# Performance work log

Measured on AMD Instinct MI355X. Metric: run time of the kernel, lower is better.

## Reference

```python
import jax, jax.numpy as jnp
import numpy as np

B, S, D, H, FF = 16, 1024, 1024, 8, 4096
DH = D // H
EPS = 1e-5

def _ln(x, g, b):
    mu = jnp.mean(x, axis=-1, keepdims=True)
    var = jnp.mean((x - mu) ** 2, axis=-1, keepdims=True)
    return (x - mu) * jax.lax.rsqrt(var + EPS) * g + b

def setup_inputs() -> dict:
    key = jax.random.key(0)
    ks = jax.random.split(key, 12)
    sd = D ** -0.5
    return {
        "x": jax.random.normal(ks[0], (B, S, D), jnp.float32),
        "bias": jax.random.normal(ks[1], (S, S), jnp.float32),
        "Wq": jax.random.normal(ks[2], (D, D), jnp.float32) * sd,
        "bq": jnp.zeros((D,), jnp.float32),
        "Wk": jax.random.normal(ks[3], (D, D), jnp.float32) * sd,
        "bk": jnp.zeros((D,), jnp.float32),
        "Wv": jax.random.normal(ks[4], (D, D), jnp.float32) * sd,
        "bv": jnp.zeros((D,), jnp.float32),
        "Wo": jax.random.normal(ks[5], (D, D), jnp.float32) * sd,
        "bo": jnp.zeros((D,), jnp.float32),
        "ln1_g": jnp.ones((D,), jnp.float32),
        "ln1_b": jnp.zeros((D,), jnp.float32),
        "W1": jax.random.normal(ks[6], (FF, D), jnp.float32) * sd,
        "b1": jnp.zeros((FF,), jnp.float32),
        "W2": jax.random.normal(ks[7], (D, FF), jnp.float32) * (FF ** -0.5),
        "b2": jnp.zeros((D,), jnp.float32),
        "ln2_g": jnp.ones((D,), jnp.float32),
        "ln2_b": jnp.zeros((D,), jnp.float32),
    }

def reference(x, bias, Wq, bq, Wk, bk, Wv, bv, Wo, bo, ln1_g, ln1_b,
              W1, b1, W2, b2, ln2_g, ln2_b):
    # torch nn.Linear: y = x @ W.T + b
    Q = x @ Wq.T + bq  # [B,S,D]
    K = x @ Wk.T + bk
    V = x @ Wv.T + bv
    # Faithful to torch: plain row-major reshape [B,S,H*dh] -> [B*H,S,dh]
    Q = Q.reshape(B * H, S, DH)
    K = K.reshape(B * H, S, DH)
    V = V.reshape(B * H, S, DH)
    scale = DH ** -0.5
    scores = jnp.einsum('bqd,bkd->bqk', Q, K)  # [B*H,S,S]
    scores = (scores + bias[None]) * scale      # bias added BEFORE scaling, as in source
    attn = jax.nn.softmax(scores, axis=-1)
    selfattention = attn[0]
    ctx = jnp.einsum('bqk,bkd->bqd', attn, V).reshape(B, S, D)
    out = ctx @ Wo.T + bo
    out = _ln(out + x, ln1_g, ln1_b)
    # FFN
    h = jax.nn.relu(out @ W1.T + b1)
    ff = h @ W2.T + b2
    out2 = _ln(ff + out, ln2_g, ln2_b)
    return out2, selfattention
```

## Files before the change

kernel.cpp:

```cpp
#include <hip/hip_runtime.h>
#include <hip/hip_bf16.h>
#include <math.h>

typedef __attribute__((ext_vector_type(4))) float f32x4;
typedef __attribute__((ext_vector_type(8))) __bf16 bf16x8;
typedef __attribute__((ext_vector_type(4))) __bf16 bf16x4;

static constexpr float SCALE = 0.08838834764831845f;
static constexpr float SCALE_LOG2E = 0.1275174482f;

__device__ __forceinline__ void load_lds16(const void* g, void* l) {
  __builtin_amdgcn_global_load_lds(
      (const __attribute__((address_space(1))) void*)g,
      (__attribute__((address_space(3))) void*)l, 16, 0, 0);
}

__global__ __launch_bounds__(256) void cast_kernel(const float* __restrict__ s,
                                                   __bf16* __restrict__ d, int n4) {
  int i = blockIdx.x * blockDim.x + threadIdx.x;
  int stride = gridDim.x * blockDim.x;
  for (; i < n4; i += stride) {
    float4 v = reinterpret_cast<const float4*>(s)[i];
    bf16x4 o;
    o[0] = (__bf16)v.x; o[1] = (__bf16)v.y; o[2] = (__bf16)v.z; o[3] = (__bf16)v.w;
    reinterpret_cast<bf16x4*>(d)[i] = o;
  }
}

__global__ __launch_bounds__(256) void scale_cast_kernel(const float* __restrict__ s,
                                                         __bf16* __restrict__ d, int n4) {
  int i = blockIdx.x * blockDim.x + threadIdx.x;
  int stride = gridDim.x * blockDim.x;
  for (; i < n4; i += stride) {
    float4 v = reinterpret_cast<const float4*>(s)[i];
    bf16x4 o;
    o[0] = (__bf16)(v.x * SCALE_LOG2E); o[1] = (__bf16)(v.y * SCALE_LOG2E);
    o[2] = (__bf16)(v.z * SCALE_LOG2E); o[3] = (__bf16)(v.w * SCALE_LOG2E);
    reinterpret_cast<bf16x4*>(d)[i] = o;
  }
}

template <int EPI>
__global__ __launch_bounds__(512, 2) void gemm_bt(
    const __bf16* __restrict__ A, const __bf16* __restrict__ Bw,
    const float* __restrict__ bvec, __bf16* __restrict__ Cb,
    float* __restrict__ Cf, int M, int N, int K) {
  __shared__ __align__(16) char sm[131072];

  const int ntn = N >> 8;
  const int nwg = gridDim.x;
  const int bid = blockIdx.x;
  const int b = (bid & 7) * (nwg >> 3) + (bid >> 3);
  const int tm = b / ntn, tn = b % ntn;
  const int t = threadIdx.x, lane = t & 63;
  const int w = t >> 6;
  const int wm = w >> 2, wn = w & 3;
  const int l15 = lane & 15, lq = lane >> 4;

  f32x4 acc[8][4] = {};

  const int r0 = t >> 3;
  const int r1 = r0 + 64;
  const int kb0 = (((t & 7) << 4) ^ ((r0 & 7) << 4));
  const int wbase = w << 10;

  auto stage = [&](int kt, int p) {
    char* base = sm + (p << 16);
    const size_t kofs = (size_t)(kb0 >> 1) + ((size_t)kt << 6);
#pragma unroll
    for (int h = 0; h < 2; ++h) {
      const __bf16* gA = A + (size_t)((tm << 8) + (h << 7) + r0) * K + kofs;
      const __bf16* gA2 = A + (size_t)((tm << 8) + (h << 7) + r1) * K + kofs;
      char* lA = base + (h << 14) + wbase;
      load_lds16(gA, lA);
      load_lds16(gA2, lA + 8192);
      const __bf16* gB = Bw + (size_t)((tn << 8) + (h << 7) + r0) * K + kofs;
      const __bf16* gB2 = Bw + (size_t)((tn << 8) + (h << 7) + r1) * K + kofs;
      char* lB = base + 32768 + (h << 14) + wbase;
      load_lds16(gB, lB);
      load_lds16(gB2, lB + 8192);
    }
  };

  stage(0, 0);
  __syncthreads();

  const int NT = K >> 6;
  const int rbB = (wn & 1) << 6;
  for (int kt = 0; kt < NT; ++kt) {
    const int p = kt & 1;
    const char* Ab = sm + (p << 16) + (wm << 14);
    const char* Bb = sm + (p << 16) + 32768 + ((wn >> 1) << 14);
    if (kt + 1 < NT) stage(kt + 1, p ^ 1);

    bf16x8 bfv[4][2];
#pragma unroll
    for (int nf = 0; nf < 4; ++nf) {
      const int r = rbB + (nf << 4) + l15;
      const int sw = (r & 7) << 4;
#pragma unroll
      for (int ks = 0; ks < 2; ++ks) {
        const int lb = (ks << 6) + (lq << 4);
        bfv[nf][ks] = *(const bf16x8*)(Bb + r * 128 + (lb ^ sw));
      }
    }
#pragma unroll
    for (int q = 0; q < 4; ++q) {
      bf16x8 af[2][2];
#pragma unroll
      for (int dm = 0; dm < 2; ++dm) {
        const int r = (((q << 1) + dm) << 4) + l15;
        const int sw = (r & 7) << 4;
#pragma unroll
        for (int ks = 0; ks < 2; ++ks) {
          const int lb = (ks << 6) + (lq << 4);
          af[dm][ks] = *(const bf16x8*)(Ab + r * 128 + (lb ^ sw));
        }
      }
#pragma unroll
      for (int ks = 0; ks < 2; ++ks)
#pragma unroll
        for (int dm = 0; dm < 2; ++dm)
#pragma unroll
          for (int nf = 0; nf < 4; ++nf)
            acc[(q << 1) + dm][nf] = __builtin_amdgcn_mfma_f32_16x16x32_bf16(
                af[dm][ks], bfv[nf][ks], acc[(q << 1) + dm][nf], 0, 0, 0);
    }
    __syncthreads();
  }

  const int row0 = (tm << 8) + (wm << 7) + (lq << 2);
  const int col0 = (tn << 8) + (wn << 6) + l15;
#pragma unroll
  for (int nf = 0; nf < 4; ++nf) {
    const int col = col0 + (nf << 4);
    const float bv = bvec[col];
#pragma unroll
    for (int mf = 0; mf < 8; ++mf) {
#pragma unroll
      for (int r = 0; r < 4; ++r) {
        const int row = row0 + (mf << 4) + r;
        float v = acc[mf][nf][r] + bv;
        if (EPI == 1) v = fmaxf(v, 0.f);
        if (EPI == 2) {
          Cf[(size_t)row * N + col] = v;
        } else if (EPI == 3) {
          size_t vt = ((size_t)(row >> 7) << 17) + ((size_t)(col & 127) << 10) +
                      ((row & 127) << 3) + (col >> 7);
          Cb[vt] = (__bf16)v;
        } else {
          Cb[(size_t)row * N + col] = (__bf16)v;
        }
      }
    }
  }
}

__global__ __launch_bounds__(256) void attn_flash(
    const __bf16* __restrict__ Q, const __bf16* __restrict__ K,
    const __bf16* __restrict__ VT, const __bf16* __restrict__ biasS,
    __bf16* __restrict__ ctx) {
  __shared__ __bf16 Ks[64 * 128];
  __shared__ __bf16 VTs[128 * 64];
  __shared__ __bf16 Ps[4][16 * 64];

  const int bid = blockIdx.x;
  const int b = ((bid & 7) << 8) | (bid >> 3);
  const int g = b >> 4;
  const int q0 = (b & 15) << 6;
  const size_t goff = (size_t)g << 17;
  const __bf16* Qg = Q + goff;
  const __bf16* Kg = K + goff;
  const __bf16* VTg = VT + goff;

  const int t = threadIdx.x, w = t >> 6, lane = t & 63;
  const int l15 = lane & 15, lq = lane >> 4;
  const int qg = q0 + (w << 4) + l15;

  bf16x8 qf[4];
  {
    const __bf16* qrow = Qg + (size_t)qg * 128 + (lq << 3);
#pragma unroll
    for (int ec = 0; ec < 4; ++ec) qf[ec] = *(const bf16x8*)(qrow + (ec << 5));
  }
  const __bf16* bSr = biasS + ((size_t)qg << 10) + (lq << 2);

  float mrun = -INFINITY, lrun = 0.f;
  f32x4 cacc[8] = {};

  for (int kb = 0; kb < 1024; kb += 64) {
    {
      int srow = lane >> 4;
      int sbo = (lane & 15) << 4;
#pragma unroll
      for (int i = 0; i < 4; ++i) {
        int c = (w << 2) + i;
        int r = (c << 2) + srow;
        int ke = (sbo ^ ((r & 7) << 4)) >> 1;
        load_lds16(Kg + (size_t)(kb + r) * 128 + ke, (char*)Ks + (c << 10));
      }
    }
    {
      int srow = lane >> 3;
      int sbo = (lane & 7) << 4;
#pragma unroll
      for (int i = 0; i < 4; ++i) {
        int c = (w << 2) + i;
        int e = (c << 3) + srow;
        int ke = kb + ((sbo ^ ((e & 7) << 4)) >> 1);
        load_lds16(VTg + (size_t)e * 1024 + ke, (char*)VTs + (c << 10));
      }
    }
    __syncthreads();

    f32x4 sacc[4] = {};
    __builtin_amdgcn_s_setprio(1);
#pragma unroll
    for (int ec = 0; ec < 4; ++ec) {
      const int lb = (ec << 6) + (lq << 4);
#pragma unroll
      for (int kn = 0; kn < 4; ++kn) {
        int rb = (kn << 4) + l15;
        bf16x8 kf = *(const bf16x8*)((const char*)Ks + rb * 256 + (lb ^ ((rb & 7) << 4)));
        sacc[kn] = __builtin_amdgcn_mfma_f32_16x16x32_bf16(kf, qf[ec], sacc[kn], 0, 0, 0);
      }
    }
    __builtin_amdgcn_s_setprio(0);

    float sv[4][4];
    const __bf16* bt = bSr + kb;
#pragma unroll
    for (int kn = 0; kn < 4; ++kn) {
      bf16x4 bb = *(const bf16x4*)(bt + (kn << 4));
#pragma unroll
      for (int r = 0; r < 4; ++r)
        sv[kn][r] = fmaf(sacc[kn][r], SCALE_LOG2E, (float)bb[r]);
    }
    float mt = sv[0][0];
#pragma unroll
    for (int kn = 0; kn < 4; ++kn)
#pragma unroll
      for (int r = 0; r < 4; ++r) mt = fmaxf(mt, sv[kn][r]);
    mt = fmaxf(mt, __shfl_xor(mt, 16));
    mt = fmaxf(mt, __shfl_xor(mt, 32));

    float alpha = 1.f;
    if (__any(mt > mrun)) {
      float mnew = fmaxf(mrun, mt);
      alpha = exp2f(mrun - mnew);
      mrun = mnew;
      float alphaR[4];
#pragma unroll
      for (int r = 0; r < 4; ++r)
        alphaR[r] = __shfl(alpha, (lane & 48) + ((lane & 48) >> 2) + r);
#pragma unroll
      for (int et = 0; et < 8; ++et)
#pragma unroll
        for (int r = 0; r < 4; ++r) cacc[et][r] *= alphaR[r];
    }
    float psum = 0.f;
#pragma unroll
    for (int kn = 0; kn < 4; ++kn)
#pragma unroll
      for (int r = 0; r < 4; ++r) {
        float p = exp2f(sv[kn][r] - mrun);
        sv[kn][r] = p;
        psum += p;
      }
    psum += __shfl_xor(psum, 16);
    psum += __shfl_xor(psum, 32);
    lrun = lrun * alpha + psum;

#pragma unroll
    for (int kn = 0; kn < 4; ++kn) {
      bf16x4 pk;
      pk[0] = (__bf16)sv[kn][0]; pk[1] = (__bf16)sv[kn][1];
      pk[2] = (__bf16)sv[kn][2]; pk[3] = (__bf16)sv[kn][3];
      int bo = (kn << 5) + (lq << 3);
      *(bf16x4*)((char*)Ps[w] + l15 * 128 + (bo ^ ((l15 & 7) << 4))) = pk;
    }
    asm volatile("s_waitcnt lgkmcnt(0)" ::: "memory");
    __builtin_amdgcn_sched_barrier(0);

    __builtin_amdgcn_s_setprio(1);
#pragma unroll
    for (int ks = 0; ks < 2; ++ks) {
      const int lb = (ks << 6) + (lq << 4);
      bf16x8 paf = *(const bf16x8*)((const char*)Ps[w] + l15 * 128 + (lb ^ ((l15 & 7) << 4)));
#pragma unroll
      for (int et = 0; et < 8; ++et) {
        int e = (et << 4) + l15;
        bf16x8 vf = *(const bf16x8*)((const char*)VTs + e * 128 + (lb ^ ((e & 7) << 4)));
        cacc[et] = __builtin_amdgcn_mfma_f32_16x16x32_bf16(paf, vf, cacc[et], 0, 0, 0);
      }
    }
    __builtin_amdgcn_s_setprio(0);
    __syncthreads();
  }

  float lrunR[4];
#pragma unroll
  for (int r = 0; r < 4; ++r)
    lrunR[r] = __shfl(lrun, (lane & 48) + ((lane & 48) >> 2) + r);
  __bf16* cg = ctx + goff;
  const int qr = q0 + (w << 4) + (lq << 2);
#pragma unroll
  for (int et = 0; et < 8; ++et)
#pragma unroll
    for (int r = 0; r < 4; ++r) {
      float v = cacc[et][r] / lrunR[r];
      cg[(size_t)(qr + r) * 128 + (et << 4) + l15] = (__bf16)v;
    }
}

__global__ __launch_bounds__(256) void attn_head0(
    const __bf16* __restrict__ Q, const __bf16* __restrict__ K,
    const float* __restrict__ bias, float* __restrict__ out) {
  __shared__ float qrow[128];
  __shared__ float red[8];
  const int q = blockIdx.x, t = threadIdx.x;
  if (t < 128) qrow[t] = (float)Q[(size_t)q * 128 + t];
  __syncthreads();
  float s[4];
#pragma unroll
  for (int c = 0; c < 4; ++c) {
    int kc = (c << 8) + t;
    const __bf16* kr = K + (size_t)kc * 128;
    float dot = 0.f;
#pragma unroll
    for (int e = 0; e < 128; e += 8) {
      bf16x8 kv = *(const bf16x8*)(kr + e);
#pragma unroll
      for (int j = 0; j < 8; ++j) dot += qrow[e + j] * (float)kv[j];
    }
    s[c] = (dot + bias[(size_t)q * 1024 + kc]) * SCALE;
  }
  float mx = fmaxf(fmaxf(s[0], s[1]), fmaxf(s[2], s[3]));
#pragma unroll
  for (int d = 32; d >= 1; d >>= 1) mx = fmaxf(mx, __shfl_xor(mx, d));
  const int w = t >> 6, lane = t & 63;
  if (lane == 0) red[w] = mx;
  __syncthreads();
  mx = fmaxf(fmaxf(red[0], red[1]), fmaxf(red[2], red[3]));
  float ex[4], sum = 0.f;
#pragma unroll
  for (int c = 0; c < 4; ++c) { ex[c] = __expf(s[c] - mx); sum += ex[c]; }
#pragma unroll
  for (int d = 32; d >= 1; d >>= 1) sum += __shfl_xor(sum, d);
  __syncthreads();
  if (lane == 0) red[4 + w] = sum;
  __syncthreads();
  sum = red[4] + red[5] + red[6] + red[7];
  float inv = 1.f / sum;
#pragma unroll
  for (int c = 0; c < 4; ++c) out[(size_t)q * 1024 + (c << 8) + t] = ex[c] * inv;
}

template <int B_BF16>
__global__ __launch_bounds__(256) void ln_res(
    const float* __restrict__ a, const void* __restrict__ bptr,
    const float* __restrict__ gam, const float* __restrict__ bet,
    float* __restrict__ outf, __bf16* __restrict__ outb) {
  __shared__ float red[8];
  const int row = blockIdx.x, t = threadIdx.x;
  const size_t base = (size_t)row << 10;
  float4 va = reinterpret_cast<const float4*>(a + base)[t];
  float b0, b1, b2, b3;
  if (B_BF16) {
    bf16x4 vb = reinterpret_cast<const bf16x4*>((const __bf16*)bptr + base)[t];
    b0 = (float)vb[0]; b1 = (float)vb[1]; b2 = (float)vb[2]; b3 = (float)vb[3];
  } else {
    float4 vb = reinterpret_cast<const float4*>((const float*)bptr + base)[t];
    b0 = vb.x; b1 = vb.y; b2 = vb.z; b3 = vb.w;
  }
  float v0 = va.x + b0, v1 = va.y + b1, v2 = va.z + b2, v3 = va.w + b3;
  float s = v0 + v1 + v2 + v3;
  float qq = v0 * v0 + v1 * v1 + v2 * v2 + v3 * v3;
#pragma unroll
  for (int d = 32; d >= 1; d >>= 1) {
    s += __shfl_xor(s, d);
    qq += __shfl_xor(qq, d);
  }
  const int w = t >> 6, lane = t & 63;
  if (lane == 0) { red[w] = s; red[4 + w] = qq; }
  __syncthreads();
  s = red[0] + red[1] + red[2] + red[3];
  qq = red[4] + red[5] + red[6] + red[7];
  const float mu = s * (1.f / 1024.f);
  const float var = qq * (1.f / 1024.f) - mu * mu;
  const float rs = rsqrtf(var + 1e-5f);
  float4 g4 = reinterpret_cast<const float4*>(gam)[t];
  float4 b4 = reinterpret_cast<const float4*>(bet)[t];
  float o0 = (v0 - mu) * rs * g4.x + b4.x;
  float o1 = (v1 - mu) * rs * g4.y + b4.y;
  float o2 = (v2 - mu) * rs * g4.z + b4.z;
  float o3 = (v3 - mu) * rs * g4.w + b4.w;
  if (outf) reinterpret_cast<float4*>(outf + base)[t] = make_float4(o0, o1, o2, o3);
  if (outb) {
    bf16x4 ob;
    ob[0] = (__bf16)o0; ob[1] = (__bf16)o1; ob[2] = (__bf16)o2; ob[3] = (__bf16)o3;
    reinterpret_cast<bf16x4*>(outb + base)[t] = ob;
  }
}

extern "C" void kernel_launch(void* const* d_in, const int* in_sizes, int n_in,
                              void* d_out, int out_size, void* d_ws, size_t ws_size,
                              hipStream_t stream) {
  (void)in_sizes; (void)n_in; (void)out_size; (void)ws_size;
  const float* x    = (const float*)d_in[0];
  const float* bias = (const float*)d_in[1];
  const float* Wq   = (const float*)d_in[2];
  const float* bq   = (const float*)d_in[3];
  const float* Wk   = (const float*)d_in[4];
  const float* bk   = (const float*)d_in[5];
  const float* Wv   = (const float*)d_in[6];
  const float* bv   = (const float*)d_in[7];
  const float* Wo   = (const float*)d_in[8];
  const float* bo   = (const float*)d_in[9];
  const float* g1   = (const float*)d_in[10];
  const float* b1l  = (const float*)d_in[11];
  const float* W1   = (const float*)d_in[12];
  const float* b1f  = (const float*)d_in[13];
  const float* W2   = (const float*)d_in[14];
  const float* b2f  = (const float*)d_in[15];
  const float* g2   = (const float*)d_in[16];
  const float* b2l  = (const float*)d_in[17];

  char* ws = (char*)d_ws;
  size_t off = 0;
  auto alloc = [&](size_t bytes) {
    char* p = ws + off;
    off += (bytes + 255) & ~(size_t)255;
    return p;
  };
  __bf16* wqb  = (__bf16*)alloc(2097152);
  __bf16* wkb  = (__bf16*)alloc(2097152);
  __bf16* wvb  = (__bf16*)alloc(2097152);
  __bf16* wob  = (__bf16*)alloc(2097152);
  __bf16* w1b  = (__bf16*)alloc(8388608);
  __bf16* w2b  = (__bf16*)alloc(8388608);
  __bf16* biasS = (__bf16*)alloc(2097152);
  __bf16* xb   = (__bf16*)alloc(33554432);
  __bf16* Qb   = (__bf16*)alloc(4ull * 33554432);
  __bf16* Kb   = Qb + 16777216;
  __bf16* VTb  = Kb + 16777216;
  __bf16* ctxb = VTb + 16777216;
  __bf16* hb   = Qb;
  __bf16* res1b = xb;

  float* out2     = (float*)d_out;
  float* selfattn = (float*)d_out + 16777216;
  float* attn_out = out2;
  float* ff       = out2;

  cast_kernel<<<2048, 256, 0, stream>>>(x, xb, 16777216 / 4);
  cast_kernel<<<1024, 256, 0, stream>>>(Wq, wqb, 1048576 / 4);
  cast_kernel<<<1024, 256, 0, stream>>>(Wk, wkb, 1048576 / 4);
  cast_kernel<<<1024, 256, 0, stream>>>(Wv, wvb, 1048576 / 4);
  cast_kernel<<<1024, 256, 0, stream>>>(Wo, wob, 1048576 / 4);
  cast_kernel<<<1024, 256, 0, stream>>>(W1, w1b, 4194304 / 4);
  cast_kernel<<<1024, 256, 0, stream>>>(W2, w2b, 4194304 / 4);
  scale_cast_kernel<<<512, 256, 0, stream>>>(bias, biasS, 1048576 / 4);

  gemm_bt<0><<<64 * 4, 512, 0, stream>>>(xb, wqb, bq, Qb, nullptr, 16384, 1024, 1024);
  gemm_bt<0><<<64 * 4, 512, 0, stream>>>(xb, wkb, bk, Kb, nullptr, 16384, 1024, 1024);
  gemm_bt<3><<<64 * 4, 512, 0, stream>>>(xb, wvb, bv, VTb, nullptr, 16384, 1024, 1024);

  attn_head0<<<1024, 256, 0, stream>>>(Qb, Kb, bias, selfattn);
  attn_flash<<<128 * 16, 256, 0, stream>>>(Qb, Kb, VTb, biasS, ctxb);

  gemm_bt<2><<<64 * 4, 512, 0, stream>>>(ctxb, wob, bo, nullptr, attn_out, 16384, 1024, 1024);

  ln_res<0><<<16384, 256, 0, stream>>>(attn_out, x, g1, b1l, nullptr, res1b);

  gemm_bt<1><<<64 * 16, 512, 0, stream>>>(res1b, w1b, b1f, hb, nullptr, 16384, 4096, 1024);
  gemm_bt<2><<<64 * 4, 512, 0, stream>>>(hb, w2b, b2f, nullptr, ff, 16384, 1024, 4096);

  ln_res<1><<<16384, 256, 0, stream>>>(ff, res1b, g2, b2l, out2, nullptr);
}
```

Measured before the change: 779.9 us.

## Double-buffer K/V tiles in flash attention and fuse weight cast launches

The flash attention kernel now keeps two LDS buffers for K and V^T and prefetches the next 64-key tile while the current one is computed. This is meant to hide global-to-LDS load latency behind the MFMA work. The s_setprio hints around the MFMA loops are removed. The six weight cast launches are merged into one kernel to cut launch overhead. LDS use per block roughly doubles for K/V, which may lower occupancy.

```diff
diff --git a/kernel.cpp b/kernel.cpp
--- a/kernel.cpp
+++ b/kernel.cpp
@@ -24,6 +24,30 @@
     bf16x4 o;
     o[0] = (__bf16)v.x; o[1] = (__bf16)v.y; o[2] = (__bf16)v.z; o[3] = (__bf16)v.w;
     reinterpret_cast<bf16x4*>(d)[i] = o;
+  }
+}
+
+__global__ __launch_bounds__(256) void cast_weights(
+    const float* __restrict__ wq, const float* __restrict__ wk,
+    const float* __restrict__ wv, const float* __restrict__ wo,
+    const float* __restrict__ w1, const float* __restrict__ w2,
+    __bf16* __restrict__ dq, __bf16* __restrict__ dk,
+    __bf16* __restrict__ dv, __bf16* __restrict__ dwo,
+    __bf16* __restrict__ d1, __bf16* __restrict__ d2) {
+  int i = blockIdx.x * blockDim.x + threadIdx.x;
+  int stride = gridDim.x * blockDim.x;
+  for (; i < 3145728; i += stride) {
+    const float* s; __bf16* d; int j;
+    if (i < 262144)       { s = wq; d = dq;  j = i; }
+    else if (i < 524288)  { s = wk; d = dk;  j = i - 262144; }
+    else if (i < 786432)  { s = wv; d = dv;  j = i - 524288; }
+    else if (i < 1048576) { s = wo; d = dwo; j = i - 786432; }
+    else if (i < 2097152) { s = w1; d = d1;  j = i - 1048576; }
+    else                  { s = w2; d = d2;  j = i - 2097152; }
+    float4 v = reinterpret_cast<const float4*>(s)[j];
+    bf16x4 o;
+    o[0] = (__bf16)v.x; o[1] = (__bf16)v.y; o[2] = (__bf16)v.z; o[3] = (__bf16)v.w;
+    reinterpret_cast<bf16x4*>(d)[j] = o;
   }
 }
 
@@ -160,8 +184,8 @@
     const __bf16* __restrict__ Q, const __bf16* __restrict__ K,
     const __bf16* __restrict__ VT, const __bf16* __restrict__ biasS,
     __bf16* __restrict__ ctx) {
-  __shared__ __bf16 Ks[64 * 128];
-  __shared__ __bf16 VTs[128 * 64];
+  __shared__ __bf16 Ks[2][64 * 128];
+  __shared__ __bf16 VTs[2][128 * 64];
   __shared__ __bf16 Ps[4][16 * 64];
 
   const int bid = blockIdx.x;
@@ -185,47 +209,57 @@
   }
   const __bf16* bSr = biasS + ((size_t)qg << 10) + (lq << 2);
 
+  auto stageK = [&](int kb, int buf) {
+    int srow = lane >> 4;
+    int sbo = (lane & 15) << 4;
+#pragma unroll
+    for (int i = 0; i < 4; ++i) {
+      int c = (w << 2) + i;
+      int r = (c << 2) + srow;
+      int ke = (sbo ^ ((r & 7) << 4)) >> 1;
+      load_lds16(Kg + (size_t)(kb + r) * 128 + ke, (char*)Ks[buf] + (c << 10));
+    }
+  };
+  auto stageV = [&](int kb, int buf) {
+    int srow = lane >> 3;
+    int sbo = (lane & 7) << 4;
+#pragma unroll
+    for (int i = 0; i < 4; ++i) {
+      int c = (w << 2) + i;
+      int e = (c << 3) + srow;
+      int ke = kb + ((sbo ^ ((e & 7) << 4)) >> 1);
+      load_lds16(VTg + (size_t)e * 1024 + ke, (char*)VTs[buf] + (c << 10));
+    }
+  };
+
   float mrun = -INFINITY, lrun = 0.f;
   f32x4 cacc[8] = {};
 
-  for (int kb = 0; kb < 1024; kb += 64) {
-    {
-      int srow = lane >> 4;
-      int sbo = (lane & 15) << 4;
-#pragma unroll
-      for (int i = 0; i < 4; ++i) {
-        int c = (w << 2) + i;
-        int r = (c << 2) + srow;
-        int ke = (sbo ^ ((r & 7) << 4)) >> 1;
-        load_lds16(Kg + (size_t)(kb + r) * 128 + ke, (char*)Ks + (c << 10));
-      }
-    }
-    {
-      int srow = lane >> 3;
-      int sbo = (lane & 7) << 4;
-#pragma unroll
-      for (int i = 0; i < 4; ++i) {
-        int c = (w << 2) + i;
-        int e = (c << 3) + srow;
-        int ke = kb + ((sbo ^ ((e & 7) << 4)) >> 1);
-        load_lds16(VTg + (size_t)e * 1024 + ke, (char*)VTs + (c << 10));
-      }
-    }
-    __syncthreads();
+  stageK(0, 0);
+  stageV(0, 0);
+  __syncthreads();
+
+  for (int it = 0; it < 16; ++it) {
+    const int kb = it << 6;
+    const int cur = it & 1;
+    if (it < 15) {
+      stageK(kb + 64, cur ^ 1);
+      stageV(kb + 64, cur ^ 1);
+    }
+    const char* Ksc = (const char*)Ks[cur];
+    const char* VTc = (const char*)VTs[cur];
 
     f32x4 sacc[4] = {};
-    __builtin_amdgcn_s_setprio(1);
 #pragma unroll
     for (int ec = 0; ec < 4; ++ec) {
       const int lb = (ec << 6) + (lq << 4);
 #pragma unroll
       for (int kn = 0; kn < 4; ++kn) {
         int rb = (kn << 4) + l15;
-        bf16x8 kf = *(const bf16x8*)((const char*)Ks + rb * 256 + (lb ^ ((rb & 7) << 4)));
+        bf16x8 kf = *(const bf16x8*)(Ksc + rb * 256 + (lb ^ ((rb & 7) << 4)));
         sacc[kn] = __builtin_amdgcn_mfma_f32_16x16x32_bf16(kf, qf[ec], sacc[kn], 0, 0, 0);
       }
     }
-    __builtin_amdgcn_s_setprio(0);
 
     float sv[4][4];
     const __bf16* bt = bSr + kb;
@@ -282,7 +316,6 @@
     asm volatile("s_waitcnt lgkmcnt(0)" ::: "memory");
     __builtin_amdgcn_sched_barrier(0);
 
-    __builtin_amdgcn_s_setprio(1);
 #pragma unroll
     for (int ks = 0; ks < 2; ++ks) {
       const int lb = (ks << 6) + (lq << 4);
@@ -290,11 +323,10 @@
 #pragma unroll
       for (int et = 0; et < 8; ++et) {
         int e = (et << 4) + l15;
-        bf16x8 vf = *(const bf16x8*)((const char*)VTs + e * 128 + (lb ^ ((e & 7) << 4)));
+        bf16x8 vf = *(const bf16x8*)(VTc + e * 128 + (lb ^ ((e & 7) << 4)));
         cacc[et] = __builtin_amdgcn_mfma_f32_16x16x32_bf16(paf, vf, cacc[et], 0, 0, 0);
       }
     }
-    __builtin_amdgcn_s_setprio(0);
     __syncthreads();
   }
 
@@ -454,12 +486,8 @@
   float* ff       = out2;
 
   cast_kernel<<<2048, 256, 0, stream>>>(x, xb, 16777216 / 4);
-  cast_kernel<<<1024, 256, 0, stream>>>(Wq, wqb, 1048576 / 4);
-  cast_kernel<<<1024, 256, 0, stream>>>(Wk, wkb, 1048576 / 4);
-  cast_kernel<<<1024, 256, 0, stream>>>(Wv, wvb, 1048576 / 4);
-  cast_kernel<<<1024, 256, 0, stream>>>(Wo, wob, 1048576 / 4);
-  cast_kernel<<<1024, 256, 0, stream>>>(W1, w1b, 4194304 / 4);
-  cast_kernel<<<1024, 256, 0, stream>>>(W2, w2b, 4194304 / 4);
+  cast_weights<<<2048, 256, 0, stream>>>(Wq, Wk, Wv, Wo, W1, W2,
+                                         wqb, wkb, wvb, wob, w1b, w2b);
   scale_cast_kernel<<<512, 256, 0, stream>>>(bias, biasS, 1048576 / 4);
 
   gemm_bt<0><<<64 * 4, 512, 0, stream>>>(xb, wqb, bq, Qb, nullptr, 16384, 1024, 1024);
```

After: 793.7 us. Within noise of the previous version (+1.8%).
